# Kernel optimization log

Measured on AMD Instinct MI355X. Metric: run time of the kernel, lower is better.

The kernel has to match this reference:

```python
import jax, jax.numpy as jnp
import numpy as np

B, T, E = 32, 100, 512
H = 640          # predictor embed/hidden dim
J = 640          # joint hidden dim
V = 4096         # vocab size; blank index == V
BLANK = V
MAX_SYMBOLS = 2  # max_symbols_per_step


def setup_inputs() -> dict:
    key = jax.random.key(0)
    ks = jax.random.split(key, 11)
    s = 0.02
    return {
        "encoder_output": jax.random.normal(ks[0], (B, E, T), jnp.float32),
        "encoded_lengths": jax.random.randint(ks[1], (B,), 0, T).astype(jnp.int32),
        "embed": jax.random.normal(ks[2], (V + 1, H), jnp.float32) * s,
        "W_i": jax.random.normal(ks[3], (H, 4 * H), jnp.float32) * s,
        "W_h": jax.random.normal(ks[4], (H, 4 * H), jnp.float32) * s,
        "b_lstm": jnp.zeros((4 * H,), jnp.float32),
        "W_enc": jax.random.normal(ks[5], (E, J), jnp.float32) * s,
        "W_pred": jax.random.normal(ks[6], (H, J), jnp.float32) * s,
        "b_joint": jnp.zeros((J,), jnp.float32),
        "W_out": jax.random.normal(ks[7], (J, V + 1), jnp.float32) * s,
        "b_out": jnp.zeros((V + 1,), jnp.float32),
    }


def _lstm_step(x, h, c, W_i, W_h, b):
    z = x @ W_i + h @ W_h + b                      # [B, 4H]
    i, f, g, o = jnp.split(z, 4, axis=-1)
    i, f, o = jax.nn.sigmoid(i), jax.nn.sigmoid(f), jax.nn.sigmoid(o)
    c = f * c + i * jnp.tanh(g)
    return o * jnp.tanh(c), c


def _greedy_decode(enc_bte, lengths, embed, W_i, W_h, b_lstm,
                   W_enc, W_pred, b_joint, W_out, b_out):
    """Batched RNNT greedy decode. Returns (labels [B,T*MS], counts [B], score [B]).
    Instead of the host-side early break when blank_mask is all-true, we run the
    bounded inner loop with per-sequence commit masking; once a sequence is blank
    its state/label/output freeze, so the per-sequence results are identical."""
    Bv = enc_bte.shape[0]
    enc_proj = enc_bte @ W_enc                     # [B, T, J] (same math as per-step enc projection)
    batch_ix = jnp.arange(Bv)

    h0 = jnp.zeros((Bv, H), enc_bte.dtype)
    c0 = jnp.zeros((Bv, H), enc_bte.dtype)
    last0 = jnp.full((Bv,), BLANK, jnp.int32)      # SOS == blank
    labels0 = jnp.full((Bv, T * MAX_SYMBOLS), BLANK, jnp.int32)
    counts0 = jnp.zeros((Bv,), jnp.int32)
    score0 = jnp.zeros((Bv,), jnp.float32)

    def inner(icarry, s_and_t):
        h, c, last_label, blank_mask, labels, counts, score = icarry
        s, t = s_and_t
        use_sos = jnp.logical_and(t == 0, s == 0)
        x = jnp.where(use_sos, 0.0, embed[last_label])      # [B, H]; SOS -> zero vector
        h1, c1 = _lstm_step(x, h, c, W_i, W_h, b_lstm)
        logits = jax.nn.relu(enc_proj[:, t] + h1 @ W_pred + b_joint) @ W_out + b_out  # [B, V+1]
        logp = jax.nn.log_softmax(logits, axis=-1)          # CPU path in original
        k = jnp.argmax(logp, axis=-1)                       # [B]
        v = jnp.take_along_axis(logp, k[:, None], axis=-1)[:, 0]
        new_blank = blank_mask | (k == BLANK)
        commit = ~new_blank                                  # only non-blank sequences advance
        cm = commit[:, None]
        h = jnp.where(cm, h1, h)
        c = jnp.where(cm, c1, c)
        k32 = k.astype(jnp.int32)
        last_label = jnp.where(commit, k32, last_label)
        labels = labels.at[batch_ix, counts].set(
            jnp.where(commit, k32, labels[batch_ix, counts]))
        counts = counts + commit.astype(jnp.int32)
        score = score + jnp.where(commit, v, 0.0)
        return (h, c, last_label, new_blank, labels, counts, score), None

    def outer(carry, t):
        h, c, last_label, labels, counts, score = carry
        blank_mask = t >= lengths                            # [B]
        icarry = (h, c, last_label, blank_mask, labels, counts, score)
        icarry, _ = jax.lax.scan(
            lambda cc, s: inner(cc, (s, t)), icarry, jnp.arange(MAX_SYMBOLS))
        h, c, last_label, _, labels, counts, score = icarry
        return (h, c, last_label, labels, counts, score), None

    carry = (h0, c0, last0, labels0, counts0, score0)
    carry, _ = jax.lax.scan(outer, carry, jnp.arange(T))
    _, _, _, labels, counts, score = carry
    return labels, counts, score


def reference(encoder_output, encoded_lengths, embed, W_i, W_h, b_lstm,
              W_enc, W_pred, b_joint, W_out, b_out):
    enc = jnp.transpose(encoder_output, (0, 2, 1))           # (B, F, T) -> (B, T, F)
    labels, counts, score = _greedy_decode(
        enc, encoded_lengths, embed, W_i, W_h, b_lstm,
        W_enc, W_pred, b_joint, W_out, b_out)
    return labels, counts, score
```

## Files before the change

kernel.cpp:

```cpp
#include <hip/hip_runtime.h>


#define NB 512
#define S1B 320
#define HRS 20480

__device__ __forceinline__ unsigned f2ord(float f) {
  unsigned u = __float_as_uint(f);
  return (u & 0x80000000u) ? ~u : (u | 0x80000000u);
}
__device__ __forceinline__ float ord2f(unsigned u) {
  return __uint_as_float((u & 0x80000000u) ? (u & 0x7fffffffu) : ~u);
}
__device__ __forceinline__ unsigned long long shfl_xor_u64(unsigned long long x, int m) {
  int lo = __shfl_xor((int)(unsigned)x, m, 64);
  int hi = __shfl_xor((int)(unsigned)(x >> 32), m, 64);
  return ((unsigned long long)(unsigned)hi << 32) | (unsigned)lo;
}

__device__ __forceinline__ void st_coh_f32(float* p, float v) {
  asm volatile("global_store_dword %0, %1, off sc0 sc1" :: "v"(p), "v"(v) : "memory");
}
__device__ __forceinline__ void st_coh_u32(unsigned* p, unsigned v) {
  asm volatile("global_store_dword %0, %1, off sc0 sc1" :: "v"(p), "v"(v) : "memory");
}
__device__ __forceinline__ unsigned ld_coh_u32(const unsigned* p) {
  unsigned r;
  asm volatile("global_load_dword %0, %1, off sc0 sc1\n\ts_waitcnt vmcnt(0)"
               : "=v"(r) : "v"(p) : "memory");
  return r;
}

__device__ __forceinline__ void gbarrier(unsigned* __restrict__ arrive,
                                         unsigned* __restrict__ go, unsigned it) {
  const int blk = blockIdx.x, tid = threadIdx.x;
  __syncthreads();
  if (blk == 0) {
    for (int f = 1 + tid; f < NB; f += 256) {
      while (ld_coh_u32(arrive + f * 4) < it) __builtin_amdgcn_s_sleep(1);
    }
    __syncthreads();
    if (tid < 64) st_coh_u32(go + tid * 4, it);
    __syncthreads();
  } else {
    if (tid == 0) {
      st_coh_u32(arrive + blk * 4, it);
      while (ld_coh_u32(go + (blk & 63) * 4) < it) __builtin_amdgcn_s_sleep(1);
    }
    __syncthreads();
  }
}

__device__ __forceinline__ void stage_tile(float (*__restrict__ t)[320],
                                           const float* __restrict__ src_row,
                                           int rb, int q) {
#pragma unroll
  for (int p = 0; p < 10; ++p) {
    int c = q + (p << 3);
    float4 v = *(const float4*)(src_row + (c << 2));
    *(float4*)&t[rb][(c ^ (rb & 7)) << 2] = v;
  }
}
__device__ __forceinline__ float4 tile_read(const float (*__restrict__ t)[320],
                                            int b, int c) {
  return *(const float4*)&t[b][(c ^ (b & 7)) << 2];
}

__global__ __launch_bounds__(256) void rnnt_prep(
    const float* __restrict__ enc, const float* __restrict__ W_i,
    const float* __restrict__ W_h, const float* __restrict__ W_pred,
    const float* __restrict__ W_out, const float* __restrict__ W_enc,
    const float* __restrict__ b_joint,
    float* __restrict__ out, float* __restrict__ Wcat_t,
    float* __restrict__ Wpred_t, float* __restrict__ Wout_k4,
    float* __restrict__ enc_projB, float* __restrict__ h_ring,
    unsigned long long* __restrict__ kslot, unsigned long long* __restrict__ sslot,
    unsigned* __restrict__ arrive, unsigned* __restrict__ go) {
  const int blk = blockIdx.x, tid = threadIdx.x;
  const int gtid = blk * 256 + tid;
  const int GT = gridDim.x * 256;
  __shared__ float s_tr[32][33];

  for (int x = gtid; x < 6464; x += GT) out[x] = (x < 6400) ? 4096.0f : 0.0f;
  for (int x = gtid; x < HRS; x += GT) h_ring[(size_t)200 * HRS + x] = 0.f;
  for (int x = gtid; x < 51200; x += GT) { kslot[x] = 0ull; sslot[x] = 0ull; }
  for (int x = gtid; x < NB * 4; x += GT) arrive[x] = 0u;
  for (int x = gtid; x < 64 * 4; x += GT) go[x] = 0u;

  {
    const int NT0 = 1600, NT1 = 1600, NT2 = 400;
    for (int tl = blk; tl < NT0 + NT1 + NT2; tl += gridDim.x) {
      const float* src; float* dst; int C, DS, DO, CT; int tt = tl;
      if (tt < NT0)               { src = W_i;    dst = Wcat_t;  C = 2560; DS = 1280; DO = 0;   CT = 80; }
      else if ((tt -= NT0) < NT1) { src = W_h;    dst = Wcat_t;  C = 2560; DS = 1280; DO = 640; CT = 80; }
      else { tt -= NT1;             src = W_pred; dst = Wpred_t; C = 640;  DS = 640;  DO = 0;   CT = 20; }
      int rt = tt / CT, ct = tt % CT;
      int r0 = rt * 32, c0 = ct * 32;
      __syncthreads();
#pragma unroll
      for (int p = 0; p < 4; ++p) {
        int rr = (tid >> 5) + 8 * p, cc = tid & 31;
        s_tr[rr][cc] = src[(r0 + rr) * C + c0 + cc];
      }
      __syncthreads();
#pragma unroll
      for (int p = 0; p < 4; ++p) {
        int cc2 = (tid >> 5) + 8 * p, rr2 = tid & 31;
        dst[(c0 + cc2) * DS + DO + r0 + rr2] = s_tr[rr2][cc2];
      }
    }
  }

  for (int g = gtid; g < 160 * 4097; g += GT) {
    int k4 = g / 4097, v = g - k4 * 4097;
    float4 o;
    o.x = W_out[(size_t)(4 * k4 + 0) * 4097 + v];
    o.y = W_out[(size_t)(4 * k4 + 1) * 4097 + v];
    o.z = W_out[(size_t)(4 * k4 + 2) * 4097 + v];
    o.w = W_out[(size_t)(4 * k4 + 3) * 4097 + v];
    ((float4*)Wout_k4)[g] = o;
  }

  for (int idx = gtid; idx < 2048000; idx += GT) {
    int b = idx / 64000, r = idx % 64000;
    int tt = r / 640, j = r % 640;
    const float* ep = enc + b * 51200;
    float acc = b_joint[j];
#pragma unroll 4
    for (int e = 0; e < 512; ++e) acc += ep[e * 100 + tt] * W_enc[e * 640 + j];
    enc_projB[idx] = acc;
  }
}

__global__ __launch_bounds__(256, 2) void rnnt_decode(
    const int* __restrict__ lens, const float* __restrict__ embed,
    const float* __restrict__ b_lstm, const float* __restrict__ b_out,
    float* __restrict__ out,
    const float* __restrict__ Wcat_t, const float* __restrict__ Wpred_t,
    const float* __restrict__ Wout_k4, const float* __restrict__ enc_projB,
    float* __restrict__ h_ring, float* __restrict__ jt_ring,
    unsigned long long* __restrict__ kslot, unsigned long long* __restrict__ sslot,
    unsigned* __restrict__ arrive, unsigned* __restrict__ go) {
  const int blk = blockIdx.x, tid = threadIdx.x;

  __shared__ float s_tile[32][320];
  __shared__ float s_zp[2][4][32][2];
  __shared__ float s_red[4][64];
  __shared__ unsigned long long s_dk[32], s_ds[32];
  __shared__ int s_last[32], s_hsrc[32], s_commit[32];

  int last_r = 4096, hsrc_r = 200, cnt_r = 0;
  bool blank_r = false;
  float score_r = 0.f;
  float c_comm = 0.f, c_cand = 0.f;
  unsigned it = 0;
  const int len_b = lens[tid & 31];

  for (int i = 0;; ++i) {
    if (i > 0) {
      int ip = i - 1;
      int b8 = tid >> 3, sl = tid & 7;
      unsigned long long kv = kslot[((size_t)ip * 32 + b8) * 8 + sl];
      unsigned long long sv = sslot[((size_t)ip * 32 + b8) * 8 + sl];
#pragma unroll
      for (int d = 1; d < 8; d <<= 1) {
        unsigned long long ok = shfl_xor_u64(kv, d);
        if (ok > kv) kv = ok;
        sv += shfl_xor_u64(sv, d);
      }
      if (sl == 0) { s_dk[b8] = kv; s_ds[b8] = sv; }
    }
    __syncthreads();
    if (tid < 32) {
      int b = tid;
      int cm = 0;
      if (i > 0) {
        unsigned long long key = s_dk[b], sum = s_ds[b];
        int kArg = 4096 - (int)(key & 0xffffffffu);
        float bl = ord2f((unsigned)(key >> 32));
        float lse = logf((float)sum * 0x1p-32f);
        float vsc = bl - lse;
        int im1 = i - 1, tp = im1 >> 1, sp = im1 & 1;
        bool blank_in = (sp == 0) ? (tp >= len_b) : blank_r;
        bool nb = blank_in || (kArg == 4096);
        blank_r = nb;
        if (!nb) {
          if (blk == b) out[b * 200 + cnt_r] = (float)kArg;
          last_r = kArg; hsrc_r = im1; cnt_r++; score_r += vsc; cm = 1;
        }
      }
      if (i == 200 && blk == b) { out[6400 + b] = (float)cnt_r; out[6432 + b] = score_r; }
      s_last[b] = last_r; s_hsrc[b] = hsrc_r; s_commit[b] = cm;
    }
    __syncthreads();
    if (i == 200) return;
    const int t = i >> 1;

    if (blk < S1B) {
      const int b = tid & 31;
      const int g = (tid >> 5) & 3;
      const int half = tid >> 7;
      const int j0 = blk * 2;
      float a0 = 0.f, a1 = 0.f, a2 = 0.f, a3 = 0.f;
      float e0 = 0.f, e1 = 0.f, e2 = 0.f, e3 = 0.f;
      if (i > 0) {
        const int rb = tid >> 3, q = tid & 7;
#pragma unroll 1
        for (int tt = 0; tt < 4; ++tt) {
          const float* src = (tt < 2)
              ? embed + (size_t)s_last[rb] * 640 + tt * 320
              : h_ring + (size_t)s_hsrc[rb] * HRS + rb * 640 + (tt - 2) * 320;
          stage_tile(s_tile, src, rb, q);
          __syncthreads();
          if ((tt >> 1) == half) {
            const float* wr = Wcat_t + (size_t)(g * 640 + j0) * 1280 +
                              half * 640 + (tt & 1) * 320;
            const float* wr2 = wr + 1280;
#pragma unroll 8
            for (int cc = 0; cc < 80; ++cc) {
              float4 xv = tile_read(s_tile, b, cc);
              float4 wa = *(const float4*)(wr + cc * 4);
              float4 wb = *(const float4*)(wr2 + cc * 4);
              a0 += wa.x * xv.x; a1 += wa.y * xv.y;
              a2 += wa.z * xv.z; a3 += wa.w * xv.w;
              e0 += wb.x * xv.x; e1 += wb.y * xv.y;
              e2 += wb.z * xv.z; e3 += wb.w * xv.w;
            }
          }
          __syncthreads();
        }
      }
      float z0 = (a0 + a1) + (a2 + a3);
      float z1 = (e0 + e1) + (e2 + e3);
      if (half == 0) { z0 += b_lstm[g * 640 + j0]; z1 += b_lstm[g * 640 + j0 + 1]; }
      s_zp[half][g][b][0] = z0;
      s_zp[half][g][b][1] = z1;
    }
    __syncthreads();
    if (blk < S1B && tid < 64) {
      const int b = tid >> 1, j_l = tid & 1;
      float zi = s_zp[0][0][b][j_l] + s_zp[1][0][b][j_l];
      float zf = s_zp[0][1][b][j_l] + s_zp[1][1][b][j_l];
      float zg = s_zp[0][2][b][j_l] + s_zp[1][2][b][j_l];
      float zo = s_zp[0][3][b][j_l] + s_zp[1][3][b][j_l];
      if (s_commit[b]) c_comm = c_cand;
      float ig = 1.f / (1.f + expf(-zi));
      float fg = 1.f / (1.f + expf(-zf));
      float og = 1.f / (1.f + expf(-zo));
      float cn = fg * c_comm + ig * tanhf(zg);
      float hn = og * tanhf(cn);
      c_cand = cn;
      st_coh_f32(&h_ring[(size_t)i * HRS + b * 640 + blk * 2 + j_l], hn);
    }
    gbarrier(arrive, go, ++it);

    if (blk < S1B) {
      const int w = tid >> 6, lane = tid & 63, bb = lane >> 1, j_l = lane & 1;
      const int j = blk * 2 + j_l;
      const int rb = tid >> 3, q = tid & 7;
      float r0 = 0.f, r1 = 0.f, r2 = 0.f, r3 = 0.f;
#pragma unroll 1
      for (int tt = 0; tt < 2; ++tt) {
        const float* src = h_ring + (size_t)i * HRS + rb * 640 + tt * 320;
        stage_tile(s_tile, src, rb, q);
        __syncthreads();
        if ((w >> 1) == tt) {
          const float* wp = Wpred_t + (size_t)j * 640 + w * 160;
          const int c0 = (w & 1) * 40;
#pragma unroll 8
          for (int cc = 0; cc < 40; ++cc) {
            float4 hv = tile_read(s_tile, bb, c0 + cc);
            float4 wv = *(const float4*)(wp + cc * 4);
            r0 += wv.x * hv.x; r1 += wv.y * hv.y;
            r2 += wv.z * hv.z; r3 += wv.w * hv.w;
          }
        }
        __syncthreads();
      }
      s_red[w][lane] = (r0 + r1) + (r2 + r3);
    }
    __syncthreads();
    if (blk < S1B && tid < 64) {
      const int b = tid >> 1, j_l = tid & 1, j = blk * 2 + j_l;
      float sm = (s_red[0][tid] + s_red[1][tid]) + (s_red[2][tid] + s_red[3][tid]);
      float val = enc_projB[(b * 100 + t) * 640 + j] + sm;
      st_coh_f32(&jt_ring[(size_t)i * HRS + b * 640 + j], fmaxf(val, 0.f));
    }
    gbarrier(arrive, go, ++it);

    {
      const int b = tid >> 3, v_l = tid & 7;
      const int v = blk * 8 + v_l;
      const int kq = v_l;
      float a0 = 0.f, a1 = 0.f, a2 = 0.f, a3 = 0.f;
      float p0 = 0.f, p1 = 0.f, p2 = 0.f, p3 = 0.f;
      const int rb = tid >> 3, q = tid & 7;
#pragma unroll 1
      for (int tt = 0; tt < 2; ++tt) {
        const float* src = jt_ring + (size_t)i * HRS + rb * 640 + tt * 320;
        stage_tile(s_tile, src, rb, q);
        __syncthreads();
        const float* wk = Wout_k4 + ((size_t)tt * 80 * 4097 + v) * 4;
#pragma unroll 8
        for (int cc = 0; cc < 80; ++cc) {
          float4 jv = tile_read(s_tile, b, cc);
          float4 wv = *(const float4*)(wk + (size_t)cc * 4097 * 4);
          a0 += wv.x * jv.x; a1 += wv.y * jv.y;
          a2 += wv.z * jv.z; a3 += wv.w * jv.w;
        }
        if (blk == NB - 1 && (kq >> 2) == tt) {
          const float* wb4 = Wout_k4 + ((size_t)(kq * 20) * 4097 + 4096) * 4;
          const int c0 = kq * 20 - tt * 80;
#pragma unroll
          for (int cc = 0; cc < 20; ++cc) {
            float4 jv = tile_read(s_tile, b, c0 + cc);
            float4 wv = *(const float4*)(wb4 + (size_t)cc * 4097 * 4);
            p0 += wv.x * jv.x; p1 += wv.y * jv.y;
            p2 += wv.z * jv.z; p3 += wv.w * jv.w;
          }
        }
        __syncthreads();
      }
      float acc = ((a0 + a1) + (a2 + a3)) + b_out[v];
      unsigned long long key =
          ((unsigned long long)f2ord(acc) << 32) | (unsigned)(4096 - v);
      unsigned long long isum =
          (unsigned long long)(expf(acc) * 4294967296.0f + 0.5f);
#pragma unroll
      for (int d = 1; d < 8; d <<= 1) {
        unsigned long long ok = shfl_xor_u64(key, d);
        if (ok > key) key = ok;
        isum += shfl_xor_u64(isum, d);
      }
      if (v_l == 0) {
        atomicMax(&kslot[((size_t)i * 32 + b) * 8 + (blk & 7)], key);
        atomicAdd(&sslot[((size_t)i * 32 + b) * 8 + (blk & 7)], isum);
      }
      if (blk == NB - 1) {
        float part = (p0 + p1) + (p2 + p3);
#pragma unroll
        for (int d = 1; d < 8; d <<= 1) part += __shfl_xor(part, d, 64);
        if (kq == 0) {
          float aB = part + b_out[4096];
          unsigned long long key2 = ((unsigned long long)f2ord(aB) << 32);
          unsigned long long is2 =
              (unsigned long long)(expf(aB) * 4294967296.0f + 0.5f);
          atomicMax(&kslot[((size_t)i * 32 + b) * 8 + 7], key2);
          atomicAdd(&sslot[((size_t)i * 32 + b) * 8 + 7], is2);
        }
      }
    }
    gbarrier(arrive, go, ++it);
  }
}

extern "C" void kernel_launch(void* const* d_in, const int* in_sizes, int n_in,
                              void* d_out, int out_size, void* d_ws, size_t ws_size,
                              hipStream_t stream) {
  (void)in_sizes; (void)n_in; (void)out_size; (void)ws_size;
  const float* enc    = (const float*)d_in[0];
  const int*   lens   = (const int*)d_in[1];
  const float* embed  = (const float*)d_in[2];
  const float* W_i    = (const float*)d_in[3];
  const float* W_h    = (const float*)d_in[4];
  const float* b_lstm = (const float*)d_in[5];
  const float* W_enc  = (const float*)d_in[6];
  const float* W_pred = (const float*)d_in[7];
  const float* b_joint= (const float*)d_in[8];
  const float* W_out  = (const float*)d_in[9];
  const float* b_out  = (const float*)d_in[10];
  float* out = (float*)d_out;

  char* ws = (char*)d_ws;
  size_t off = 0;
  auto carve = [&](size_t bytes) -> void* {
    void* p = ws + off;
    off += (bytes + 255) & ~(size_t)255;
    return p;
  };
  unsigned* arrive           = (unsigned*)carve((size_t)NB * 4 * 4);
  unsigned* go               = (unsigned*)carve((size_t)64 * 4 * 4);
  unsigned long long* kslot  = (unsigned long long*)carve((size_t)51200 * 8);
  unsigned long long* sslot  = (unsigned long long*)carve((size_t)51200 * 8);
  float* h_ring   = (float*)carve((size_t)201 * HRS * 4);
  float* jt_ring  = (float*)carve((size_t)200 * HRS * 4);
  float* Wpred_t  = (float*)carve((size_t)640 * 640 * 4);
  float* Wcat_t   = (float*)carve((size_t)2560 * 1280 * 4);
  float* Wout_k4  = (float*)carve((size_t)160 * 4097 * 16);
  float* enc_projB= (float*)carve((size_t)32 * 100 * 640 * 4);

  rnnt_prep<<<2048, 256, 0, stream>>>(
      enc, W_i, W_h, W_pred, W_out, W_enc, b_joint,
      out, Wcat_t, Wpred_t, Wout_k4, enc_projB, h_ring, kslot, sslot, arrive, go);
  rnnt_decode<<<NB, 256, 0, stream>>>(
      lens, embed, b_lstm, b_out, out,
      Wcat_t, Wpred_t, Wout_k4, enc_projB, h_ring, jt_ring, kslot, sslot,
      arrive, go);
}
```

Before: 15.70 ms.

## Keep per-block W_out columns resident in LDS and halve staging tile width

W_out is now transposed to a [4097,640] layout in the prep kernel. Each decode block loads its 8 vocab columns plus the blank column into shared memory once, so the joint output projection reads weights from LDS on every step instead of global memory. The shared activation tile shrinks from 320 to 160 columns to make room, which doubles the number of stage/sync rounds in the LSTM, predictor and joint loops. The grid barrier's master block also polls two arrive flags per thread in one batched load, replacing the sequential spin loop.

Result: no change. 15.66 ms (-0.3%).

```diff
diff --git a/kernel.cpp b/kernel.cpp
--- a/kernel.cpp
+++ b/kernel.cpp
@@ -30,15 +30,25 @@
                : "=v"(r) : "v"(p) : "memory");
   return r;
 }
+__device__ __forceinline__ bool poll2(const unsigned* p1, const unsigned* p2,
+                                      unsigned it) {
+  unsigned r1, r2;
+  asm volatile("global_load_dword %0, %2, off sc0 sc1\n\t"
+               "global_load_dword %1, %3, off sc0 sc1\n\t"
+               "s_waitcnt vmcnt(0)"
+               : "=v"(r1), "=v"(r2) : "v"(p1), "v"(p2) : "memory");
+  return (r1 >= it) && (r2 >= it);
+}
 
 __device__ __forceinline__ void gbarrier(unsigned* __restrict__ arrive,
                                          unsigned* __restrict__ go, unsigned it) {
   const int blk = blockIdx.x, tid = threadIdx.x;
   __syncthreads();
   if (blk == 0) {
-    for (int f = 1 + tid; f < NB; f += 256) {
-      while (ld_coh_u32(arrive + f * 4) < it) __builtin_amdgcn_s_sleep(1);
-    }
+    int f1 = 1 + tid; if (f1 > 511) f1 = 511;
+    int f2 = 257 + tid; if (f2 > 511) f2 = 511;
+    while (!poll2(arrive + f1 * 4, arrive + f2 * 4, it))
+      __builtin_amdgcn_s_sleep(1);
     __syncthreads();
     if (tid < 64) st_coh_u32(go + tid * 4, it);
     __syncthreads();
@@ -51,17 +61,17 @@
   }
 }
 
-__device__ __forceinline__ void stage_tile(float (*__restrict__ t)[320],
+__device__ __forceinline__ void stage_tile(float (*__restrict__ t)[160],
                                            const float* __restrict__ src_row,
                                            int rb, int q) {
 #pragma unroll
-  for (int p = 0; p < 10; ++p) {
+  for (int p = 0; p < 5; ++p) {
     int c = q + (p << 3);
     float4 v = *(const float4*)(src_row + (c << 2));
     *(float4*)&t[rb][(c ^ (rb & 7)) << 2] = v;
   }
 }
-__device__ __forceinline__ float4 tile_read(const float (*__restrict__ t)[320],
+__device__ __forceinline__ float4 tile_read(const float (*__restrict__ t)[160],
                                             int b, int c) {
   return *(const float4*)&t[b][(c ^ (b & 7)) << 2];
 }
@@ -72,7 +82,7 @@
     const float* __restrict__ W_out, const float* __restrict__ W_enc,
     const float* __restrict__ b_joint,
     float* __restrict__ out, float* __restrict__ Wcat_t,
-    float* __restrict__ Wpred_t, float* __restrict__ Wout_k4,
+    float* __restrict__ Wpred_t, float* __restrict__ Wout_t,
     float* __restrict__ enc_projB, float* __restrict__ h_ring,
     unsigned long long* __restrict__ kslot, unsigned long long* __restrict__ sslot,
     unsigned* __restrict__ arrive, unsigned* __restrict__ go) {
@@ -88,37 +98,30 @@
   for (int x = gtid; x < 64 * 4; x += GT) go[x] = 0u;
 
   {
-    const int NT0 = 1600, NT1 = 1600, NT2 = 400;
-    for (int tl = blk; tl < NT0 + NT1 + NT2; tl += gridDim.x) {
+    const int NT0 = 1600, NT1 = 1600, NT2 = 400, NT3 = 2580;
+    for (int tl = blk; tl < NT0 + NT1 + NT2 + NT3; tl += gridDim.x) {
       const float* src; float* dst; int C, DS, DO, CT; int tt = tl;
       if (tt < NT0)               { src = W_i;    dst = Wcat_t;  C = 2560; DS = 1280; DO = 0;   CT = 80; }
       else if ((tt -= NT0) < NT1) { src = W_h;    dst = Wcat_t;  C = 2560; DS = 1280; DO = 640; CT = 80; }
-      else { tt -= NT1;             src = W_pred; dst = Wpred_t; C = 640;  DS = 640;  DO = 0;   CT = 20; }
+      else if ((tt -= NT1) < NT2) { src = W_pred; dst = Wpred_t; C = 640;  DS = 640;  DO = 0;   CT = 20; }
+      else { tt -= NT2;             src = W_out;  dst = Wout_t;  C = 4097; DS = 640;  DO = 0;   CT = 129; }
       int rt = tt / CT, ct = tt % CT;
       int r0 = rt * 32, c0 = ct * 32;
       __syncthreads();
 #pragma unroll
       for (int p = 0; p < 4; ++p) {
         int rr = (tid >> 5) + 8 * p, cc = tid & 31;
-        s_tr[rr][cc] = src[(r0 + rr) * C + c0 + cc];
+        float v = 0.f;
+        if (c0 + cc < C) v = src[(r0 + rr) * C + c0 + cc];
+        s_tr[rr][cc] = v;
       }
       __syncthreads();
 #pragma unroll
       for (int p = 0; p < 4; ++p) {
         int cc2 = (tid >> 5) + 8 * p, rr2 = tid & 31;
-        dst[(c0 + cc2) * DS + DO + r0 + rr2] = s_tr[rr2][cc2];
-      }
-    }
-  }
-
-  for (int g = gtid; g < 160 * 4097; g += GT) {
-    int k4 = g / 4097, v = g - k4 * 4097;
-    float4 o;
-    o.x = W_out[(size_t)(4 * k4 + 0) * 4097 + v];
-    o.y = W_out[(size_t)(4 * k4 + 1) * 4097 + v];
-    o.z = W_out[(size_t)(4 * k4 + 2) * 4097 + v];
-    o.w = W_out[(size_t)(4 * k4 + 3) * 4097 + v];
-    ((float4*)Wout_k4)[g] = o;
+        if (c0 + cc2 < C) dst[(c0 + cc2) * DS + DO + r0 + rr2] = s_tr[rr2][cc2];
+      }
+    }
   }
 
   for (int idx = gtid; idx < 2048000; idx += GT) {
@@ -137,17 +140,25 @@
     const float* __restrict__ b_lstm, const float* __restrict__ b_out,
     float* __restrict__ out,
     const float* __restrict__ Wcat_t, const float* __restrict__ Wpred_t,
-    const float* __restrict__ Wout_k4, const float* __restrict__ enc_projB,
+    const float* __restrict__ Wout_t, const float* __restrict__ enc_projB,
     float* __restrict__ h_ring, float* __restrict__ jt_ring,
     unsigned long long* __restrict__ kslot, unsigned long long* __restrict__ sslot,
     unsigned* __restrict__ arrive, unsigned* __restrict__ go) {
   const int blk = blockIdx.x, tid = threadIdx.x;
 
-  __shared__ float s_tile[32][320];
+  __shared__ float s_tile[32][160];
+  __shared__ float s_wout[9 * 640];
   __shared__ float s_zp[2][4][32][2];
   __shared__ float s_red[4][64];
   __shared__ unsigned long long s_dk[32], s_ds[32];
   __shared__ int s_last[32], s_hsrc[32], s_commit[32];
+
+  for (int x = tid; x < 9 * 160; x += 256) {
+    int col = x / 160, cc = x - col * 160;
+    int vcol = (col < 8) ? blk * 8 + col : 4096;
+    *(float4*)&s_wout[col * 640 + cc * 4] =
+        *(const float4*)(Wout_t + (size_t)vcol * 640 + cc * 4);
+  }
 
   int last_r = 4096, hsrc_r = 200, cnt_r = 0;
   bool blank_r = false;
@@ -206,18 +217,18 @@
       if (i > 0) {
         const int rb = tid >> 3, q = tid & 7;
 #pragma unroll 1
-        for (int tt = 0; tt < 4; ++tt) {
-          const float* src = (tt < 2)
-              ? embed + (size_t)s_last[rb] * 640 + tt * 320
-              : h_ring + (size_t)s_hsrc[rb] * HRS + rb * 640 + (tt - 2) * 320;
+        for (int tt = 0; tt < 8; ++tt) {
+          const float* src = (tt < 4)
+              ? embed + (size_t)s_last[rb] * 640 + tt * 160
+              : h_ring + (size_t)s_hsrc[rb] * HRS + rb * 640 + (tt - 4) * 160;
           stage_tile(s_tile, src, rb, q);
           __syncthreads();
-          if ((tt >> 1) == half) {
+          if ((tt >> 2) == half) {
             const float* wr = Wcat_t + (size_t)(g * 640 + j0) * 1280 +
-                              half * 640 + (tt & 1) * 320;
+                              half * 640 + (tt & 3) * 160;
             const float* wr2 = wr + 1280;
 #pragma unroll 8
-            for (int cc = 0; cc < 80; ++cc) {
+            for (int cc = 0; cc < 40; ++cc) {
               float4 xv = tile_read(s_tile, b, cc);
               float4 wa = *(const float4*)(wr + cc * 4);
               float4 wb = *(const float4*)(wr2 + cc * 4);
@@ -260,16 +271,15 @@
       const int rb = tid >> 3, q = tid & 7;
       float r0 = 0.f, r1 = 0.f, r2 = 0.f, r3 = 0.f;
 #pragma unroll 1
-      for (int tt = 0; tt < 2; ++tt) {
-        const float* src = h_ring + (size_t)i * HRS + rb * 640 + tt * 320;
+      for (int tt = 0; tt < 4; ++tt) {
+        const float* src = h_ring + (size_t)i * HRS + rb * 640 + tt * 160;
         stage_tile(s_tile, src, rb, q);
         __syncthreads();
-        if ((w >> 1) == tt) {
+        if (w == tt) {
           const float* wp = Wpred_t + (size_t)j * 640 + w * 160;
-          const int c0 = (w & 1) * 40;
 #pragma unroll 8
           for (int cc = 0; cc < 40; ++cc) {
-            float4 hv = tile_read(s_tile, bb, c0 + cc);
+            float4 hv = tile_read(s_tile, bb, cc);
             float4 wv = *(const float4*)(wp + cc * 4);
             r0 += wv.x * hv.x; r1 += wv.y * hv.y;
             r2 += wv.z * hv.z; r3 += wv.w * hv.w;
@@ -296,25 +306,25 @@
       float p0 = 0.f, p1 = 0.f, p2 = 0.f, p3 = 0.f;
       const int rb = tid >> 3, q = tid & 7;
 #pragma unroll 1
-      for (int tt = 0; tt < 2; ++tt) {
-        const float* src = jt_ring + (size_t)i * HRS + rb * 640 + tt * 320;
+      for (int tt = 0; tt < 4; ++tt) {
+        const float* src = jt_ring + (size_t)i * HRS + rb * 640 + tt * 160;
         stage_tile(s_tile, src, rb, q);
         __syncthreads();
-        const float* wk = Wout_k4 + ((size_t)tt * 80 * 4097 + v) * 4;
+        const float* wk = s_wout + v_l * 640 + tt * 160;
 #pragma unroll 8
-        for (int cc = 0; cc < 80; ++cc) {
+        for (int cc = 0; cc < 40; ++cc) {
           float4 jv = tile_read(s_tile, b, cc);
-          float4 wv = *(const float4*)(wk + (size_t)cc * 4097 * 4);
+          float4 wv = *(const float4*)(wk + cc * 4);
           a0 += wv.x * jv.x; a1 += wv.y * jv.y;
           a2 += wv.z * jv.z; a3 += wv.w * jv.w;
         }
-        if (blk == NB - 1 && (kq >> 2) == tt) {
-          const float* wb4 = Wout_k4 + ((size_t)(kq * 20) * 4097 + 4096) * 4;
-          const int c0 = kq * 20 - tt * 80;
+        if (blk == NB - 1 && (kq >> 1) == tt) {
+          const float* wb4 = s_wout + 8 * 640 + kq * 80;
+          const int c0 = (kq & 1) * 20;
 #pragma unroll
           for (int cc = 0; cc < 20; ++cc) {
             float4 jv = tile_read(s_tile, b, c0 + cc);
-            float4 wv = *(const float4*)(wb4 + (size_t)cc * 4097 * 4);
+            float4 wv = *(const float4*)(wb4 + cc * 4);
             p0 += wv.x * jv.x; p1 += wv.y * jv.y;
             p2 += wv.z * jv.z; p3 += wv.w * jv.w;
           }
@@ -386,14 +396,14 @@
   float* jt_ring  = (float*)carve((size_t)200 * HRS * 4);
   float* Wpred_t  = (float*)carve((size_t)640 * 640 * 4);
   float* Wcat_t   = (float*)carve((size_t)2560 * 1280 * 4);
-  float* Wout_k4  = (float*)carve((size_t)160 * 4097 * 16);
+  float* Wout_t   = (float*)carve((size_t)4097 * 640 * 4);
   float* enc_projB= (float*)carve((size_t)32 * 100 * 640 * 4);
 
   rnnt_prep<<<2048, 256, 0, stream>>>(
       enc, W_i, W_h, W_pred, W_out, W_enc, b_joint,
-      out, Wcat_t, Wpred_t, Wout_k4, enc_projB, h_ring, kslot, sslot, arrive, go);
+      out, Wcat_t, Wpred_t, Wout_t, enc_projB, h_ring, kslot, sslot, arrive, go);
   rnnt_decode<<<NB, 256, 0, stream>>>(
       lens, embed, b_lstm, b_out, out,
-      Wcat_t, Wpred_t, Wout_k4, enc_projB, h_ring, jt_ring, kslot, sslot,
+      Wcat_t, Wpred_t, Wout_t, enc_projB, h_ring, jt_ring, kslot, sslot,
       arrive, go);
 }
```
